# Kernel tuning notes

Measured on AMD Instinct MI355X. Metric: run time of the kernel, lower is better.

The kernel has to match this reference:

```python
import jax, jax.numpy as jnp
import numpy as np

B, S, HID, H = 8, 1024, 1024, 16
D = HID // H  # dim per head = 64

def setup_inputs() -> dict:
    key = jax.random.key(0)
    ks = jax.random.split(key, 7)
    s = 1.0 / np.sqrt(D)  # mimic nn.Linear uniform init scale
    return {
        "sequences": jax.random.normal(ks[0], (B, S, HID), dtype=jnp.float32),
        "Wq": jax.random.uniform(ks[1], (H, D, D), jnp.float32, -s, s),
        "bq": jax.random.uniform(ks[2], (H, D), jnp.float32, -s, s),
        "Wk": jax.random.uniform(ks[3], (H, D, D), jnp.float32, -s, s),
        "bk": jax.random.uniform(ks[4], (H, D), jnp.float32, -s, s),
        "Wv": jax.random.uniform(ks[5], (H, D, D), jnp.float32, -s, s),
        "bv": jax.random.uniform(ks[6], (H, D), jnp.float32, -s, s),
    }

def reference(sequences, Wq, bq, Wk, bk, Wv, bv):
    # per-head input slice h is sequences[:, :, h*D:(h+1)*D] == reshape
    x = sequences.reshape(B, S, H, D)
    # torch Linear: y = x @ W.T + b, W is [out, in] -> einsum 'bshd,hed->bshe'
    q = jnp.einsum('bshd,hed->bshe', x, Wq) + bq
    k = jnp.einsum('bshd,hed->bshe', x, Wk) + bk
    v = jnp.einsum('bshd,hed->bshe', x, Wv) + bv
    scores = jnp.einsum('bshe,bthe->bhst', q, k) / jnp.sqrt(jnp.float32(D))
    attn = jax.nn.softmax(scores, axis=-1)  # [B,H,S,S]
    out = jnp.einsum('bhst,bthe->bshe', attn, v)
    return out.reshape(B, S, HID)  # hstack of heads == reshape
```

## Files before the change

### kernel.cpp

```cpp
#include <hip/hip_runtime.h>
#include <hip/hip_bf16.h>

#define B_   8
#define S_   1024
#define HID_ 1024
#define H_   16
#define D_   64

typedef __hip_bfloat16 bf16;
typedef __attribute__((ext_vector_type(8))) short s16x8;
typedef __attribute__((ext_vector_type(4))) float f32x4;

#define QK_BH 65536
#define V_BH  65536

__device__ __forceinline__ short f2b(float f) {
    union { float f; unsigned u; } a; a.f = f;
    return (short)((a.u + 0x8000u) >> 16);
}
__device__ __forceinline__ s16x8 cvt8(const float* p) {
    const float4* q = (const float4*)p;
    float4 u = q[0], v = q[1];
    s16x8 r;
    r[0] = f2b(u.x); r[1] = f2b(u.y); r[2] = f2b(u.z); r[3] = f2b(u.w);
    r[4] = f2b(v.x); r[5] = f2b(v.y); r[6] = f2b(v.z); r[7] = f2b(v.w);
    return r;
}
__device__ __forceinline__ s16x8 load8bf(const bf16* p) {
    return *(const s16x8*)p;
}

__global__ __launch_bounds__(256) void cvt_w(
    const float* __restrict__ Wq, const float* __restrict__ Wk,
    const float* __restrict__ Wv, bf16* __restrict__ Wf)
{
    const float* srcs[3] = {Wq, Wk, Wv};
    const float* src = srcs[blockIdx.y];
    bf16* dst = Wf + (size_t)blockIdx.y * (H_ * D_ * D_);
    const int i = blockIdx.x * 256 + threadIdx.x;
    const int h = i >> 9;
    const int r = i & 511;
    const int et = r >> 7, half = (r >> 6) & 1, lane = r & 63;
    const int quad = lane >> 4, c = lane & 15;
    const float* s = src + h * 4096 + (et * 16 + c) * 64 + half * 32 + quad * 8;
    bf16* d = dst + h * 4096 + et * 1024 + half * 512 + lane * 8;
    *(s16x8*)d = cvt8(s);
}

__global__ __launch_bounds__(256) void qkv_proj(
    const float* __restrict__ x, const bf16* __restrict__ Wf,
    const float* __restrict__ bq, const float* __restrict__ bk,
    const float* __restrict__ bv,
    bf16* __restrict__ Qf, bf16* __restrict__ Kf, bf16* __restrict__ Vf)
{
    __shared__ __align__(16) bf16 xs[64][72];

    const int id = blockIdx.x;
    const int bh_i = id & 127, sc = id >> 7;
    const int b = bh_i >> 4, h = bh_i & 15;
    const int t = threadIdx.x;
    const int wave = t >> 6, lane = t & 63;
    const int quad = lane >> 4, c = lane & 15;
    const size_t bh = (size_t)bh_i;

    {
        const float* xg = x + ((size_t)b * S_ + sc * 64) * HID_ + h * D_;
#pragma unroll
        for (int i = 0; i < 4; ++i) {
            const int j = i * 256 + t;
            const int row = j >> 4, seg = j & 15;
            float4 v = *(const float4*)(xg + (size_t)row * HID_ + seg * 4);
            short4 pk;
            pk.x = f2b(v.x); pk.y = f2b(v.y); pk.z = f2b(v.z); pk.w = f2b(v.w);
            *(short4*)&xs[row][seg * 4] = pk;
        }
    }
    __syncthreads();

    s16x8 xa0 = *(const s16x8*)&xs[wave * 16 + c][quad * 8];
    s16x8 xa1 = *(const s16x8*)&xs[wave * 16 + c][32 + quad * 8];

    const float* bs[3] = {bq, bk, bv};

#pragma unroll
    for (int m = 0; m < 3; ++m) {
        const bf16*  Wm   = Wf + ((size_t)m * H_ + h) * 4096;
        const float* bias = bs[m] + h * D_;
#pragma unroll
        for (int et = 0; et < 4; ++et) {
            s16x8 wf0 = load8bf(Wm + et * 1024 + lane * 8);
            s16x8 wf1 = load8bf(Wm + et * 1024 + 512 + lane * 8);
            if (m < 2) {
                const int hp = et >> 1;
                const int qp = (2 * et + (quad >> 1)) & 3;
                const float4 bb = *(const float4*)&bias[et * 16 + quad * 4];
                f32x4 acc = {0.f, 0.f, 0.f, 0.f};
                acc = __builtin_amdgcn_mfma_f32_16x16x32_bf16(wf0, xa0, acc, 0, 0, 0);
                acc = __builtin_amdgcn_mfma_f32_16x16x32_bf16(wf1, xa1, acc, 0, 0, 0);
                const int ts = sc * 4 + wave;
                bf16* dst = (m == 0 ? Qf : Kf) + bh * QK_BH + ts * 1024 +
                            hp * 512 + (qp * 16 + c) * 8 + (quad & 1) * 4;
                short4 pk;
                pk.x = f2b(acc[0] + bb.x);
                pk.y = f2b(acc[1] + bb.y);
                pk.z = f2b(acc[2] + bb.z);
                pk.w = f2b(acc[3] + bb.w);
                *(short4*)dst = pk;
            } else {
                const float bbv = bias[et * 16 + c];
                f32x4 acc = {0.f, 0.f, 0.f, 0.f};
                acc = __builtin_amdgcn_mfma_f32_16x16x32_bf16(xa0, wf0, acc, 0, 0, 0);
                acc = __builtin_amdgcn_mfma_f32_16x16x32_bf16(xa1, wf1, acc, 0, 0, 0);
                bf16* dst = Vf + bh * V_BH + sc * 4096 + et * 1024 +
                            (wave >> 1) * 512 + (quad * 16 + c) * 8 + (wave & 1) * 4;
                short4 pk;
                pk.x = f2b(acc[0] + bbv);
                pk.y = f2b(acc[1] + bbv);
                pk.z = f2b(acc[2] + bbv);
                pk.w = f2b(acc[3] + bbv);
                *(short4*)dst = pk;
            }
        }
    }
}

__global__ __launch_bounds__(256, 2) void attn(
    const bf16* __restrict__ Qf, const bf16* __restrict__ Kf,
    const bf16* __restrict__ Vf, float* __restrict__ out)
{
    __shared__ __align__(16) float os[4][16][68];

    const int id = blockIdx.x;
    const int bh_i = id & 127, qc = id >> 7;
    const int b = bh_i >> 4, h = bh_i & 15;
    const int wave = threadIdx.x >> 6, lane = threadIdx.x & 63;
    const int quad = lane >> 4, c = lane & 15;
    const int ts0 = qc * 16 + wave * 4;
    const size_t bh = (size_t)bh_i;

    s16x8 aq[4][2];
#pragma unroll
    for (int mt = 0; mt < 4; ++mt) {
        const bf16* Qb = Qf + bh * QK_BH + (ts0 + mt) * 1024 + lane * 8;
        aq[mt][0] = load8bf(Qb);
        aq[mt][1] = load8bf(Qb + 512);
    }

    f32x4 o[4][4];
#pragma unroll
    for (int mt = 0; mt < 4; ++mt)
#pragma unroll
        for (int et = 0; et < 4; ++et) o[mt][et] = {0.f, 0.f, 0.f, 0.f};
    float l[4] = {0.f, 0.f, 0.f, 0.f};

    const float CEXP = 0.18033688011112042f;
    const float NM0  = -16.0f * 0.18033688011112042f;

    const bf16* Kb = Kf + bh * QK_BH + lane * 8;
    const bf16* Vb = Vf + bh * V_BH  + lane * 8;

#pragma unroll 1
    for (int kt = 0; kt < S_ / 64; ++kt) {
        s16x8 ka[4], kb2[4];
#pragma unroll
        for (int ct = 0; ct < 4; ++ct) {
            ka[ct]  = load8bf(Kb + (kt * 4 + ct) * 1024);
            kb2[ct] = load8bf(Kb + (kt * 4 + ct) * 1024 + 512);
        }
        s16x8 vf4[4][2];
#pragma unroll
        for (int et = 0; et < 4; ++et)
#pragma unroll
            for (int p = 0; p < 2; ++p)
                vf4[et][p] = load8bf(Vb + kt * 4096 + et * 1024 + p * 512);

#pragma unroll
        for (int mt = 0; mt < 4; ++mt) {
            f32x4 s[4];
#pragma unroll
            for (int ct = 0; ct < 4; ++ct) {
                f32x4 acc = {0.f, 0.f, 0.f, 0.f};
                acc = __builtin_amdgcn_mfma_f32_16x16x32_bf16(ka[ct],  aq[mt][0], acc, 0, 0, 0);
                acc = __builtin_amdgcn_mfma_f32_16x16x32_bf16(kb2[ct], aq[mt][1], acc, 0, 0, 0);
                s[ct] = acc;
            }
            s16x8 pz[2];
#pragma unroll
            for (int p = 0; p < 2; ++p) {
                s16x8 z;
#pragma unroll
                for (int j = 0; j < 4; ++j) {
                    float pa = __builtin_amdgcn_exp2f(fmaf(s[2 * p][j],     CEXP, NM0));
                    float pb = __builtin_amdgcn_exp2f(fmaf(s[2 * p + 1][j], CEXP, NM0));
                    l[mt] += pa + pb;
                    z[j]     = f2b(pa);
                    z[4 + j] = f2b(pb);
                }
                pz[p] = z;
            }
#pragma unroll
            for (int et = 0; et < 4; ++et) {
                o[mt][et] = __builtin_amdgcn_mfma_f32_16x16x32_bf16(pz[0], vf4[et][0], o[mt][et], 0, 0, 0);
                o[mt][et] = __builtin_amdgcn_mfma_f32_16x16x32_bf16(pz[1], vf4[et][1], o[mt][et], 0, 0, 0);
            }
        }
    }

#pragma unroll
    for (int mt = 0; mt < 4; ++mt) {
        float L = l[mt];
        L += __shfl_xor(L, 16, 64);
        L += __shfl_xor(L, 32, 64);
        const float Linv = 1.0f / L;
        float inv[4];
#pragma unroll
        for (int r = 0; r < 4; ++r)
            inv[r] = __shfl(Linv, quad * 4 + r, 64);
#pragma unroll
        for (int et = 0; et < 4; ++et)
#pragma unroll
            for (int r = 0; r < 4; ++r)
                os[wave][quad * 4 + r][et * 16 + c] = o[mt][et][r] * inv[r];
        float* orow = out + ((size_t)b * S_ + (ts0 + mt) * 16 + c) * HID_ + h * D_;
#pragma unroll
        for (int j = 0; j < 4; ++j) {
            float4 v = *(const float4*)&os[wave][c][(quad + j * 4) * 4];
            *(float4*)(orow + (quad + j * 4) * 4) = v;
        }
    }
}

extern "C" void kernel_launch(void* const* d_in, const int* in_sizes, int n_in,
                              void* d_out, int out_size, void* d_ws, size_t ws_size,
                              hipStream_t stream) {
    (void)in_sizes; (void)n_in; (void)out_size; (void)ws_size;
    const float* x  = (const float*)d_in[0];
    const float* Wq = (const float*)d_in[1];
    const float* bq = (const float*)d_in[2];
    const float* Wk = (const float*)d_in[3];
    const float* bk = (const float*)d_in[4];
    const float* Wv = (const float*)d_in[5];
    const float* bv = (const float*)d_in[6];
    float* outp = (float*)d_out;

    bf16* Qfw = (bf16*)d_ws;
    bf16* Kfw = Qfw + (size_t)128 * QK_BH;
    bf16* Vfw = Kfw + (size_t)128 * QK_BH;
    bf16* Wfw = Vfw + (size_t)128 * V_BH;

    cvt_w<<<dim3(32, 3), 256, 0, stream>>>(Wq, Wk, Wv, Wfw);
    qkv_proj<<<dim3(2048), 256, 0, stream>>>(x, Wfw, bq, bk, bv, Qfw, Kfw, Vfw);
    attn<<<dim3(512), 256, 0, stream>>>(Qfw, Kfw, Vfw, outp);
}
```

Measured before the change: 149.2 us.

## Double-buffer K/V tiles in LDS via async global_load_lds and MFMA row sums

Each 64-key tile of K and V is now staged into a double-buffered shared-memory region with async global-to-LDS loads, and the next tile is prefetched while the current one is computed, so global latency overlaps with MFMA work. Before this, every wave loaded the same K/V fragments from global memory on its own. The softmax denominator is now accumulated with an extra MFMA against a ones vector, which replaces the scalar sum and the cross-lane shuffles, and the bf16 packing uses v_cvt_pk_bf16_f32. The cost is a block barrier per iteration, extra LDS use that may lower occupancy, and two extra MFMAs per row tile. The denominator now sums bf16-rounded probabilities instead of fp32 ones.

```diff
diff --git a/kernel.cpp b/kernel.cpp
--- a/kernel.cpp
+++ b/kernel.cpp
@@ -28,6 +28,18 @@
 }
 __device__ __forceinline__ s16x8 load8bf(const bf16* p) {
     return *(const s16x8*)p;
+}
+
+__device__ __forceinline__ unsigned cvtpk_bf16(float lo, float hi) {
+    unsigned r;
+    asm("v_cvt_pk_bf16_f32 %0, %1, %2" : "=v"(r) : "v"(lo), "v"(hi));
+    return r;
+}
+
+typedef __attribute__((address_space(1))) const void gvoid_t;
+typedef __attribute__((address_space(3))) void lvoid_t;
+__device__ __forceinline__ void gload_lds16(const bf16* g, bf16* l) {
+    __builtin_amdgcn_global_load_lds((gvoid_t*)g, (lvoid_t*)l, 16, 0, 0);
 }
 
 __global__ __launch_bounds__(256) void cvt_w(
@@ -128,7 +140,10 @@
     const bf16* __restrict__ Qf, const bf16* __restrict__ Kf,
     const bf16* __restrict__ Vf, float* __restrict__ out)
 {
-    __shared__ __align__(16) float os[4][16][68];
+    __shared__ __align__(16) union {
+        bf16  kv[2][8192];
+        float os[4][16][68];
+    } sm;
 
     const int id = blockIdx.x;
     const int bh_i = id & 127, qc = id >> 7;
@@ -146,85 +161,113 @@
         aq[mt][1] = load8bf(Qb + 512);
     }
 
+    const f32x4 zero4 = {0.f, 0.f, 0.f, 0.f};
     f32x4 o[4][4];
-#pragma unroll
-    for (int mt = 0; mt < 4; ++mt)
-#pragma unroll
-        for (int et = 0; et < 4; ++et) o[mt][et] = {0.f, 0.f, 0.f, 0.f};
-    float l[4] = {0.f, 0.f, 0.f, 0.f};
+    f32x4 ld4[4];
+#pragma unroll
+    for (int mt = 0; mt < 4; ++mt) {
+        ld4[mt] = zero4;
+#pragma unroll
+        for (int et = 0; et < 4; ++et) o[mt][et] = zero4;
+    }
+
+    s16x8 ones;
+#pragma unroll
+    for (int j = 0; j < 8; ++j) ones[j] = (short)0x3F80;
 
     const float CEXP = 0.18033688011112042f;
     const float NM0  = -16.0f * 0.18033688011112042f;
 
-    const bf16* Kb = Kf + bh * QK_BH + lane * 8;
-    const bf16* Vb = Vf + bh * V_BH  + lane * 8;
-
+    const bf16* Kg = Kf + bh * QK_BH;
+    const bf16* Vg = Vf + bh * V_BH;
+
+    auto STAGE = [&](int kt, int bi) {
+#pragma unroll
+        for (int i = 0; i < 4; ++i) {
+            const int ch = wave * 4 + i;
+            const bf16* src = (ch < 8
+                ? Kg + (size_t)kt * 4096 + ch * 512
+                : Vg + (size_t)kt * 4096 + (ch - 8) * 512) + lane * 8;
+            gload_lds16(src, &sm.kv[bi][ch * 512]);
+        }
+    };
+
+    STAGE(0, 0);
+    __syncthreads();
+
+    int cur = 0;
 #pragma unroll 1
     for (int kt = 0; kt < S_ / 64; ++kt) {
+        if (kt < S_ / 64 - 1) STAGE(kt + 1, cur ^ 1);
+
+        const bf16* kb = &sm.kv[cur][0];
+        const bf16* vb = &sm.kv[cur][4096];
+
         s16x8 ka[4], kb2[4];
 #pragma unroll
         for (int ct = 0; ct < 4; ++ct) {
-            ka[ct]  = load8bf(Kb + (kt * 4 + ct) * 1024);
-            kb2[ct] = load8bf(Kb + (kt * 4 + ct) * 1024 + 512);
+            ka[ct]  = load8bf(kb + ct * 1024 + lane * 8);
+            kb2[ct] = load8bf(kb + ct * 1024 + 512 + lane * 8);
         }
         s16x8 vf4[4][2];
 #pragma unroll
         for (int et = 0; et < 4; ++et)
 #pragma unroll
             for (int p = 0; p < 2; ++p)
-                vf4[et][p] = load8bf(Vb + kt * 4096 + et * 1024 + p * 512);
+                vf4[et][p] = load8bf(vb + et * 1024 + p * 512 + lane * 8);
 
 #pragma unroll
         for (int mt = 0; mt < 4; ++mt) {
-            f32x4 s[4];
+            f32x4 s4[4];
 #pragma unroll
             for (int ct = 0; ct < 4; ++ct) {
-                f32x4 acc = {0.f, 0.f, 0.f, 0.f};
+                f32x4 acc = zero4;
                 acc = __builtin_amdgcn_mfma_f32_16x16x32_bf16(ka[ct],  aq[mt][0], acc, 0, 0, 0);
                 acc = __builtin_amdgcn_mfma_f32_16x16x32_bf16(kb2[ct], aq[mt][1], acc, 0, 0, 0);
-                s[ct] = acc;
+                s4[ct] = acc;
             }
             s16x8 pz[2];
 #pragma unroll
             for (int p = 0; p < 2; ++p) {
-                s16x8 z;
+                float pa[4], pb[4];
 #pragma unroll
                 for (int j = 0; j < 4; ++j) {
-                    float pa = __builtin_amdgcn_exp2f(fmaf(s[2 * p][j],     CEXP, NM0));
-                    float pb = __builtin_amdgcn_exp2f(fmaf(s[2 * p + 1][j], CEXP, NM0));
-                    l[mt] += pa + pb;
-                    z[j]     = f2b(pa);
-                    z[4 + j] = f2b(pb);
+                    pa[j] = __builtin_amdgcn_exp2f(fmaf(s4[2 * p][j],     CEXP, NM0));
+                    pb[j] = __builtin_amdgcn_exp2f(fmaf(s4[2 * p + 1][j], CEXP, NM0));
                 }
-                pz[p] = z;
-            }
+                union { unsigned u[4]; s16x8 v; } z;
+                z.u[0] = cvtpk_bf16(pa[0], pa[1]);
+                z.u[1] = cvtpk_bf16(pa[2], pa[3]);
+                z.u[2] = cvtpk_bf16(pb[0], pb[1]);
+                z.u[3] = cvtpk_bf16(pb[2], pb[3]);
+                pz[p] = z.v;
+            }
+            ld4[mt] = __builtin_amdgcn_mfma_f32_16x16x32_bf16(pz[0], ones, ld4[mt], 0, 0, 0);
+            ld4[mt] = __builtin_amdgcn_mfma_f32_16x16x32_bf16(pz[1], ones, ld4[mt], 0, 0, 0);
 #pragma unroll
             for (int et = 0; et < 4; ++et) {
                 o[mt][et] = __builtin_amdgcn_mfma_f32_16x16x32_bf16(pz[0], vf4[et][0], o[mt][et], 0, 0, 0);
                 o[mt][et] = __builtin_amdgcn_mfma_f32_16x16x32_bf16(pz[1], vf4[et][1], o[mt][et], 0, 0, 0);
             }
         }
+        __syncthreads();
+        cur ^= 1;
     }
 
 #pragma unroll
     for (int mt = 0; mt < 4; ++mt) {
-        float L = l[mt];
-        L += __shfl_xor(L, 16, 64);
-        L += __shfl_xor(L, 32, 64);
-        const float Linv = 1.0f / L;
         float inv[4];
 #pragma unroll
-        for (int r = 0; r < 4; ++r)
-            inv[r] = __shfl(Linv, quad * 4 + r, 64);
+        for (int r = 0; r < 4; ++r) inv[r] = 1.0f / ld4[mt][r];
 #pragma unroll
         for (int et = 0; et < 4; ++et)
 #pragma unroll
             for (int r = 0; r < 4; ++r)
-                os[wave][quad * 4 + r][et * 16 + c] = o[mt][et][r] * inv[r];
+                sm.os[wave][quad * 4 + r][et * 16 + c] = o[mt][et][r] * inv[r];
         float* orow = out + ((size_t)b * S_ + (ts0 + mt) * 16 + c) * HID_ + h * D_;
 #pragma unroll
         for (int j = 0; j < 4; ++j) {
-            float4 v = *(const float4*)&os[wave][c][(quad + j * 4) * 4];
+            float4 v = *(const float4*)&sm.os[wave][c][(quad + j * 4) * 4];
             *(float4*)(orow + (quad + j * 4) * 4) = v;
         }
     }
```

After: 146.2 us. -2.0%, faster.
